# Optimization experiments

Hardware: AMD Instinct MI355X
Metric: run time of the kernel (lower is better)

Reference implementation:

```python
import jax, jax.numpy as jnp
import numpy as np

B, S, H, W, C = 1, 14, 56, 56, 192
WS = 7            # cubic window
SH = 3            # shift
HEADS = 6
HD = C // HEADS
N = WS ** 3       # 343 tokens per window
NW = (S // WS) * (H // WS) * (W // WS)  # 128 windows
SCALE = HD ** -0.5
HID = 4 * C
TBL = (2 * WS - 1) ** 3  # 2197


def _rel_index():
    # faithful to torch: meshgrid with indexing='xy' and the (3*ws-1)/(2*ws-1) strides
    c = np.stack(np.meshgrid(np.arange(WS), np.arange(WS), np.arange(WS), indexing='xy'))
    f = c.reshape(3, -1)                      # (3, N)
    r = (f[:, :, None] - f[:, None, :]).transpose(1, 2, 0)  # (N, N, 3)
    r = r + (WS - 1)
    r[..., 0] *= 3 * WS - 1
    r[..., 1] *= 2 * WS - 1
    return jnp.asarray(r.sum(-1), dtype=jnp.int32)  # (N, N)

REL_IDX = _rel_index()


def _ln(x, g, b):
    m = x.mean(-1, keepdims=True)
    v = ((x - m) ** 2).mean(-1, keepdims=True)
    return (x - m) * jax.lax.rsqrt(v + 1e-5) * g + b


def _partition(x):  # (B,S,H,W,C) -> (B*nW, N, C)
    x = x.reshape(B, S // WS, WS, H // WS, WS, W // WS, WS, C)
    x = x.transpose(0, 1, 3, 5, 2, 4, 6, 7)
    return x.reshape(-1, N, C)


def _reverse(w):  # (B*nW, N, C) -> (B,S,H,W,C)
    x = w.reshape(B, S // WS, H // WS, W // WS, WS, WS, WS, C)
    x = x.transpose(0, 1, 4, 2, 5, 3, 6, 7)
    return x.reshape(B, S, H, W, C)


def setup_inputs() -> dict:
    key = jax.random.key(0)
    ks = jax.random.split(key, 16)
    L = S * H * W
    p = lambda k, shp, s=0.02: (jax.random.normal(k, shp, dtype=jnp.float32) * s)
    return {
        'x': jax.random.normal(ks[0], (B, L, C), dtype=jnp.float32),
        'mask_matrix': jax.random.normal(ks[1], (NW, N, N), dtype=jnp.float32),
        'skip': jax.random.normal(ks[2], (B, L, C), dtype=jnp.float32),
        'x_up': jax.random.normal(ks[3], (B, L, C), dtype=jnp.float32),
        'norm1_g': jnp.ones((C,), jnp.float32),
        'norm1_b': jnp.zeros((C,), jnp.float32),
        'kv_w': p(ks[4], (C, 2 * C)),
        'kv_b': jnp.zeros((2 * C,), jnp.float32),
        'rel_bias_table': p(ks[5], (TBL, HEADS)),
        'proj_w': p(ks[6], (C, C)),
        'proj_b': jnp.zeros((C,), jnp.float32),
        'norm2_g': jnp.ones((C,), jnp.float32),
        'norm2_b': jnp.zeros((C,), jnp.float32),
        'fc1_w': p(ks[7], (C, HID)),
        'fc1_b': jnp.zeros((HID,), jnp.float32),
        'fc2_w': p(ks[8], (HID, C)),
        'fc2_b': jnp.zeros((C,), jnp.float32),
    }


def reference(x, mask_matrix, skip, x_up, norm1_g, norm1_b, kv_w, kv_b,
              rel_bias_table, proj_w, proj_b, norm2_g, norm2_b,
              fc1_w, fc1_b, fc2_w, fc2_b):
    shortcut = x
    sk = _ln(skip, norm1_g, norm1_b).reshape(B, S, H, W, C)
    xu = _ln(x_up, norm1_g, norm1_b).reshape(B, S, H, W, C)
    # cyclic shift (shift_size > 0, dims divisible by window -> no padding)
    sk = jnp.roll(sk, (-SH, -SH, -SH), axis=(1, 2, 3))
    xu = jnp.roll(xu, (-SH, -SH, -SH), axis=(1, 2, 3))
    sk_w = _partition(sk)   # (Bw, N, C)
    xu_w = _partition(xu)
    Bw = sk_w.shape[0]
    kv = (sk_w @ kv_w + kv_b).reshape(Bw, N, 2, HEADS, HD)
    k = kv[:, :, 0].transpose(0, 2, 1, 3)   # (Bw, h, N, d)
    v = kv[:, :, 1].transpose(0, 2, 1, 3)
    q = xu_w.reshape(Bw, N, HEADS, HD).transpose(0, 2, 1, 3) * SCALE
    attn = jnp.einsum('bhnd,bhmd->bhnm', q, k)
    bias = rel_bias_table[REL_IDX].transpose(2, 0, 1)  # (h, N, N)
    attn = attn + bias[None]
    attn = attn.reshape(B, NW, HEADS, N, N) + mask_matrix[None, :, None]
    attn = jax.nn.softmax(attn.reshape(Bw, HEADS, N, N), axis=-1)
    out = jnp.einsum('bhnm,bhmd->bhnd', attn, v)
    out = out.transpose(0, 2, 1, 3).reshape(Bw, N, C)
    out = out @ proj_w + proj_b
    xr = _reverse(out)
    xr = jnp.roll(xr, (SH, SH, SH), axis=(1, 2, 3)).reshape(B, S * H * W, C)
    x = shortcut + xr
    h = _ln(x, norm2_g, norm2_b)
    h = jax.nn.gelu(h @ fc1_w + fc1_b, approximate=False) @ fc2_w + fc2_b
    return x + h
```

## Files before the change

### kernel.cpp

```cpp
#include <hip/hip_runtime.h>
#include <cstddef>

typedef unsigned short u16;
typedef unsigned int   u32;
typedef __bf16 bf16_t;
typedef bf16_t bf16x8 __attribute__((ext_vector_type(8)));
typedef short  s16x4  __attribute__((ext_vector_type(4)));
typedef float  f32x4  __attribute__((ext_vector_type(4)));
typedef u16    u16x4  __attribute__((ext_vector_type(4)));

#define NPAD 352
#define VTS  352

__device__ __forceinline__ u16 f2b(float f) {
  return __builtin_bit_cast(u16, (__bf16)f);
}
__device__ __forceinline__ float b2f(u16 h) {
  return __uint_as_float(((u32)h) << 16);
}
__device__ __forceinline__ f32x4 mfma16(bf16x8 a, bf16x8 b, f32x4 c) {
  return __builtin_amdgcn_mfma_f32_16x16x32_bf16(a, b, c, 0, 0, 0);
}
__device__ __forceinline__ f32x4 mfma16x16(s16x4 a, s16x4 b, f32x4 c) {
#if __has_builtin(__builtin_amdgcn_mfma_f32_16x16x16bf16_1k)
  return __builtin_amdgcn_mfma_f32_16x16x16bf16_1k(a, b, c, 0, 0, 0);
#else
  f32x4 d;
  asm volatile("v_mfma_f32_16x16x16_bf16 %0, %1, %2, %3"
               : "=&v"(d) : "v"(a), "v"(b), "v"(c));
  return d;
#endif
}
__device__ __forceinline__ void gl_lds16(const void* g, void* l) {
  __builtin_amdgcn_global_load_lds((const __attribute__((address_space(1))) void*)g,
                                   (__attribute__((address_space(3))) void*)l, 16, 0, 0);
}

__device__ __forceinline__ int win_to_global(int w, int n) {
  int ws = w >> 6, wh = (w >> 3) & 7, ww = w & 7;
  int ts = (n * 1338) >> 16;
  int rem = n - ts * 49;
  int th = (rem * 9363) >> 16;
  int tw = rem - th * 7;
  int gs = ws * 7 + ts + 3; if (gs >= 14) gs -= 14;
  int gh = wh * 7 + th + 3; if (gh >= 56) gh -= 56;
  int gw = ww * 7 + tw + 3; if (gw >= 56) gw -= 56;
  return (gs * 56 + gh) * 56 + gw;
}

#define MC_END 15488
#define LN_END (MC_END + 10976)
#define WC_END (LN_END + 1824)
#define PRE_GRID (WC_END + 726)

__global__ __launch_bounds__(256) void k_pre(
    const float* __restrict__ mask, u16* __restrict__ mb,
    const float* __restrict__ skip, const float* __restrict__ xup,
    const float* __restrict__ g1, const float* __restrict__ b1,
    u16* __restrict__ skw, u16* __restrict__ qb,
    const float* __restrict__ kv_w, const float* __restrict__ proj_w,
    const float* __restrict__ fc1_w, const float* __restrict__ fc2_w,
    u16* kvT, u16* projT, u16* fc1T, u16* fc2T,
    const float* __restrict__ tbl, u16* __restrict__ bf) {
  int bid = blockIdx.x, tid = threadIdx.x;
  if (bid < MC_END) {
    int t = bid * 256 + tid;
    int w = t / (352 * 88);
    int r = t - w * (352 * 88);
    int n = r / 88;
    int q = r - n * 88;
    u16x4 v = {0, 0, 0, 0};
    if (n < 343) {
      const float* src = mask + ((size_t)w * 343 + n) * 343 + q * 4;
      #pragma unroll
      for (int j = 0; j < 4; ++j) if (q * 4 + j < 343) v[j] = f2b(src[j]);
    }
    *(u16x4*)&mb[((size_t)w * 352 + n) * 352 + q * 4] = v;
  } else if (bid < LN_END) {
    int wid = tid >> 6, lane = tid & 63;
    int m = (bid - MC_END) * 4 + wid;
    u32 w = ((u32)m * 48914u) >> 24;
    int n = m - (int)w * 343;
    int g = win_to_global((int)w, n);
    float xs[3], xu[3];
    float s1 = 0.f, s2 = 0.f, t1 = 0.f, t2 = 0.f;
    #pragma unroll
    for (int i = 0; i < 3; ++i) {
      int c = lane + i * 64;
      xs[i] = skip[(size_t)g * 192 + c];
      xu[i] = xup[(size_t)g * 192 + c];
      s1 += xs[i]; s2 += xs[i] * xs[i];
      t1 += xu[i]; t2 += xu[i] * xu[i];
    }
    #pragma unroll
    for (int off = 1; off < 64; off <<= 1) {
      s1 += __shfl_xor(s1, off); s2 += __shfl_xor(s2, off);
      t1 += __shfl_xor(t1, off); t2 += __shfl_xor(t2, off);
    }
    const float inv = 1.f / 192.f;
    float ms = s1 * inv, vs = s2 * inv - ms * ms;
    float mu = t1 * inv, vu = t2 * inv - mu * mu;
    float rs = rsqrtf(vs + 1e-5f), ru = rsqrtf(vu + 1e-5f);
    #pragma unroll
    for (int i = 0; i < 3; ++i) {
      int c = lane + i * 64;
      float gg = g1[c], bb = b1[c];
      skw[(size_t)m * 192 + c] = f2b((xs[i] - ms) * rs * gg + bb);
      float qv = ((xu[i] - mu) * ru * gg + bb) * 0.17677669529663687f;
      int h = c >> 5, d = c & 31;
      qb[(size_t)(((int)w * 6 + h) * NPAD + n) * 32 + d] = f2b(qv);
    }
  } else if (bid < WC_END) {
    int t = (bid - LN_END) * 256 + tid;
    if (t < 384 * 192) { int nn = t / 192, kk = t - nn * 192; kvT[t] = f2b(kv_w[kk * 384 + nn]); return; }
    t -= 384 * 192;
    if (t < 256 * 192) { int nn = t / 192, kk = t - nn * 192; projT[t] = (nn < 192) ? f2b(proj_w[kk * 192 + nn]) : (u16)0; return; }
    t -= 256 * 192;
    if (t < 768 * 192) { int nn = t / 192, kk = t - nn * 192; fc1T[t] = f2b(fc1_w[kk * 768 + nn]); return; }
    t -= 768 * 192;
    if (t < 256 * 768) { int nn = t / 768, kk = t - nn * 768; fc2T[t] = (nn < 192) ? f2b(fc2_w[kk * 192 + nn]) : (u16)0; return; }
  } else {
    int t = (bid - WC_END) * 256 + tid;
    int h = t / (352 * 88);
    int r = t - h * (352 * 88);
    int n = r / 88;
    int q = r - n * 88;
    u16x4 v = {0, 0, 0, 0};
    if (n < 343 && h < 6) {
      int tsn = (n * 1338) >> 16, remn = n - tsn * 49, thn = (remn * 9363) >> 16, twn = remn - thn * 7;
      #pragma unroll
      for (int j = 0; j < 4; ++j) {
        int m = q * 4 + j;
        if (m < 343) {
          int tsm = (m * 1338) >> 16, remm = m - tsm * 49, thm = (remm * 9363) >> 16, twm = remm - thm * 7;
          int idx = (thn - thm) * 20 + (tsn - tsm) * 13 + (twn - twm) + 204;
          v[j] = f2b(tbl[idx * 6 + h]);
        }
      }
    }
    if (h < 6) *(u16x4*)&bf[((size_t)h * 352 + n) * 352 + q * 4] = v;
  }
}

__global__ __launch_bounds__(256) void k_ln2(const float* __restrict__ xr,
    const float* __restrict__ g2, const float* __restrict__ b2, u16* __restrict__ o) {
  int wid = threadIdx.x >> 6, lane = threadIdx.x & 63;
  int m = blockIdx.x * 4 + wid;
  float v[3]; float s1 = 0.f, s2 = 0.f;
  #pragma unroll
  for (int i = 0; i < 3; ++i) {
    int c = lane + i * 64;
    v[i] = xr[(size_t)m * 192 + c];
    s1 += v[i]; s2 += v[i] * v[i];
  }
  #pragma unroll
  for (int off = 1; off < 64; off <<= 1) { s1 += __shfl_xor(s1, off); s2 += __shfl_xor(s2, off); }
  const float inv = 1.f / 192.f;
  float ms = s1 * inv, vs = s2 * inv - ms * ms;
  float rs = rsqrtf(vs + 1e-5f);
  #pragma unroll
  for (int i = 0; i < 3; ++i) {
    int c = lane + i * 64;
    o[(size_t)m * 192 + c] = f2b((v[i] - ms) * rs * g2[c] + b2[c]);
  }
}

template<int EPI>
__global__ __launch_bounds__(256) void k_gemm(
    const u16* __restrict__ A, const u16* __restrict__ Bm, int K, int nbn,
    const float* __restrict__ bias,
    u16* __restrict__ outa, u16* __restrict__ outb,
    const float* __restrict__ xin, float* __restrict__ xres,
    float* __restrict__ outf) {
  __shared__ __align__(16) u16 As[128 * 32];
  __shared__ __align__(16) u16 Bs[128 * 32];
  int bid = blockIdx.x;
  int xcd = bid & 7, j = bid >> 3;
  int bn = j % nbn, bmL = j / nbn;
  int bm = xcd * 43 + bmL;
  if (bm >= 343) return;
  int tid = threadIdx.x;
  int wid = tid >> 6, lane = tid & 63, lr = lane & 15, lg = lane >> 4;
  int wr = wid >> 1, wc = wid & 1;
  f32x4 acc[4][4] = {};
  const u16* Abase = A + (size_t)bm * 128 * K;
  const u16* Bbase = Bm + (size_t)bn * 128 * K;
  int nk = K >> 5;
  for (int kt = 0; kt < nk; ++kt) {
    int ci0 = tid, ci1 = tid + 256;
    int r0 = ci0 >> 2, c0 = (ci0 & 3) * 8;
    int r1 = ci1 >> 2, c1 = (ci1 & 3) * 8;
    gl_lds16(Abase + (size_t)r0 * K + kt * 32 + c0, &As[ci0 * 8]);
    gl_lds16(Abase + (size_t)r1 * K + kt * 32 + c1, &As[ci1 * 8]);
    gl_lds16(Bbase + (size_t)r0 * K + kt * 32 + c0, &Bs[ci0 * 8]);
    gl_lds16(Bbase + (size_t)r1 * K + kt * 32 + c1, &Bs[ci1 * 8]);
    __syncthreads();
    bf16x8 af[4], bfr[4];
    #pragma unroll
    for (int mi = 0; mi < 4; ++mi) af[mi] = *(const bf16x8*)&As[(wr * 64 + mi * 16 + lr) * 32 + lg * 8];
    #pragma unroll
    for (int ni = 0; ni < 4; ++ni) bfr[ni] = *(const bf16x8*)&Bs[(wc * 64 + ni * 16 + lr) * 32 + lg * 8];
    #pragma unroll
    for (int mi = 0; mi < 4; ++mi)
      #pragma unroll
      for (int ni = 0; ni < 4; ++ni)
        acc[mi][ni] = mfma16(af[mi], bfr[ni], acc[mi][ni]);
    __syncthreads();
  }
  #pragma unroll
  for (int mi = 0; mi < 4; ++mi) {
    #pragma unroll
    for (int r = 0; r < 4; ++r) {
      int grow = bm * 128 + wr * 64 + mi * 16 + lg * 4 + r;
      if (EPI == 0) {
        u32 w = ((u32)grow * 48914u) >> 24; int n = grow - (int)w * 343;
        #pragma unroll
        for (int ni = 0; ni < 4; ++ni) {
          int gcol = bn * 128 + wc * 64 + ni * 16 + lr;
          float v = acc[mi][ni][r] + bias[gcol];
          if (gcol < 192) {
            int hh = gcol >> 5, d = gcol & 31;
            int dswz = ((((d >> 3) ^ ((n >> 1) & 3)) << 3) | (d & 7));
            outa[(size_t)(((int)w * 6 + hh) * NPAD + n) * 32 + dswz] = f2b(v);
          } else {
            int c2 = gcol - 192; int hh = c2 >> 5, d = c2 & 31;
            int nswz = ((((n >> 3) ^ ((d >> 1) & 3)) << 3) | (n & 7));
            outb[(size_t)(((int)w * 6 + hh) * 32 + d) * VTS + nswz] = f2b(v);
          }
        }
      } else if (EPI == 1) {
        #pragma unroll
        for (int ni = 0; ni < 4; ++ni) {
          int gcol = bn * 128 + wc * 64 + ni * 16 + lr;
          if (gcol < 192) {
            float v = acc[mi][ni][r] + bias[gcol] + xin[(size_t)grow * 192 + gcol];
            xres[(size_t)grow * 192 + gcol] = v;
          }
        }
      } else if (EPI == 2) {
        #pragma unroll
        for (int ni = 0; ni < 4; ++ni) {
          int gcol = bn * 128 + wc * 64 + ni * 16 + lr;
          float v = acc[mi][ni][r] + bias[gcol];
          v = 0.5f * v * (1.f + erff(v * 0.7071067811865476f));
          outa[(size_t)grow * 768 + gcol] = f2b(v);
        }
      } else {
        #pragma unroll
        for (int ni = 0; ni < 4; ++ni) {
          int gcol = bn * 128 + wc * 64 + ni * 16 + lr;
          if (gcol < 192)
            outf[(size_t)grow * 192 + gcol] = acc[mi][ni][r] + bias[gcol] + xin[(size_t)grow * 192 + gcol];
        }
      }
    }
  }
}

template<int CT0, int LEN>
__device__ __forceinline__ void pf_load(const u16* __restrict__ brow, const u16* __restrict__ mrow,
                                        u16x4* bb, u16x4* mm) {
  #pragma unroll
  for (int j = 0; j < LEN; ++j) {
    bb[j] = *(const u16x4*)&brow[(CT0 + j) * 16];
    mm[j] = *(const u16x4*)&mrow[(CT0 + j) * 16];
  }
}

template<int CT0, int LEN, bool TAIL>
__device__ __forceinline__ void attn_chunk(const u16* __restrict__ Ks, const u16* __restrict__ Vs,
    bf16x8 qa, int lr, int lg, int swz, const u16x4* bb, const u16x4* mm,
    f32x4& o0, f32x4& o1, float& mrun, float& sum) {
  f32x4 s[LEN];
  const f32x4 z = {0.f, 0.f, 0.f, 0.f};
  __builtin_amdgcn_s_setprio(1);
  #pragma unroll
  for (int j = 0; j < LEN; ++j) {
    bf16x8 kf = *(const bf16x8*)&Ks[((CT0 + j) * 16 + lr) * 32 + (lg ^ swz) * 8];
    s[j] = mfma16(kf, qa, z);
  }
  __builtin_amdgcn_s_setprio(0);
  #pragma unroll
  for (int j = 0; j < LEN; ++j)
    #pragma unroll
    for (int r = 0; r < 4; ++r) s[j][r] += b2f(bb[j][r]) + b2f(mm[j][r]);
  if (TAIL) {
    int m0 = 336 + lg * 4;
    #pragma unroll
    for (int r = 0; r < 4; ++r) if (m0 + r >= 343) s[LEN - 1][r] = -1e30f;
  }
  float mloc = -1e30f;
  #pragma unroll
  for (int j = 0; j < LEN; ++j)
    mloc = fmaxf(mloc, fmaxf(fmaxf(s[j][0], s[j][1]), fmaxf(s[j][2], s[j][3])));
  mloc = fmaxf(mloc, __shfl_xor(mloc, 16));
  mloc = fmaxf(mloc, __shfl_xor(mloc, 32));
  float mnew = fmaxf(mrun, mloc);
  float scale = __expf(mrun - mnew);
  #pragma unroll
  for (int r = 0; r < 4; ++r) { o0[r] *= scale; o1[r] *= scale; }
  sum *= scale;
  float lsum = 0.f;
  #pragma unroll
  for (int j = 0; j < LEN; ++j)
    #pragma unroll
    for (int r = 0; r < 4; ++r) { float p = __expf(s[j][r] - mnew); s[j][r] = p; lsum += p; }
  lsum += __shfl_xor(lsum, 16);
  lsum += __shfl_xor(lsum, 32);
  sum += lsum;
  mrun = mnew;
  __builtin_amdgcn_s_setprio(1);
  #pragma unroll
  for (int j = 0; j < LEN; ++j) {
    s16x4 pa;
    #pragma unroll
    for (int r = 0; r < 4; ++r) pa[r] = (short)f2b(s[j][r]);
    int c16 = 2 * (CT0 + j) + (lg >> 1);
    int vo = ((c16 ^ swz) * 8) + (lg & 1) * 4;
    s16x4 v0 = *(const s16x4*)&Vs[lr * 352 + vo];
    s16x4 v1 = *(const s16x4*)&Vs[(16 + lr) * 352 + vo];
    o0 = mfma16x16(pa, v0, o0);
    o1 = mfma16x16(pa, v1, o1);
  }
  __builtin_amdgcn_s_setprio(0);
}

__global__ __launch_bounds__(256, 2) void k_attn(const u16* __restrict__ qb, const u16* __restrict__ kb,
    const u16* __restrict__ vtb, const u16* __restrict__ bfull, const u16* __restrict__ maskbf,
    u16* __restrict__ att) {
  __shared__ __align__(16) u16 Ks[352 * 32];
  __shared__ __align__(16) u16 Vs[32 * 352];
  __shared__ __align__(16) u16 Ot[4][16][40];
  int bid = blockIdx.x;
  int xcd = bid & 7, i = bid >> 3;
  int wl = i / 6, h = i - wl * 6;
  int w = xcd * 16 + wl;
  int tid = threadIdx.x, wid = tid >> 6, lane = tid & 63, lr = lane & 15, lg = lane >> 4;
  const u16* Q  = qb  + (size_t)(w * 6 + h) * NPAD * 32;
  const u16* Kg = kb  + (size_t)(w * 6 + h) * NPAD * 32;
  const u16* Vg = vtb + (size_t)(w * 6 + h) * 32 * VTS;
  const u16* Bp = bfull + (size_t)h * 352 * 352;
  const u16* Mp = maskbf + (size_t)w * 352 * 352;
  #pragma unroll
  for (int it = 0; it < 11; ++it) {
    int idx = it * 256 + tid;
    if (idx < 1408) gl_lds16(Kg + idx * 8, &Ks[idx * 8]);
    else            gl_lds16(Vg + (idx - 1408) * 8, &Vs[(idx - 1408) * 8]);
  }
  __syncthreads();
  int swz = (lr >> 1) & 3;
  for (int rt = wid; rt < 22; rt += 4) {
    int n = rt * 16 + lr;
    bf16x8 qa = *(const bf16x8*)&Q[(size_t)n * 32 + lg * 8];
    const u16* brow = Bp + (size_t)n * 352 + lg * 4;
    const u16* mrow = Mp + (size_t)n * 352 + lg * 4;
    f32x4 o0 = {0.f, 0.f, 0.f, 0.f}, o1 = {0.f, 0.f, 0.f, 0.f};
    float mrun = -1e30f, sum = 0.f;
    u16x4 bbA[6], mmA[6], bbB[6], mmB[6];
    pf_load<0, 6>(brow, mrow, bbA, mmA);
    pf_load<6, 6>(brow, mrow, bbB, mmB);
    attn_chunk<0, 6, false>(Ks, Vs, qa, lr, lg, swz, bbA, mmA, o0, o1, mrun, sum);
    pf_load<12, 6>(brow, mrow, bbA, mmA);
    attn_chunk<6, 6, false>(Ks, Vs, qa, lr, lg, swz, bbB, mmB, o0, o1, mrun, sum);
    pf_load<18, 4>(brow, mrow, bbB, mmB);
    attn_chunk<12, 6, false>(Ks, Vs, qa, lr, lg, swz, bbA, mmA, o0, o1, mrun, sum);
    attn_chunk<18, 4, true>(Ks, Vs, qa, lr, lg, swz, bbB, mmB, o0, o1, mrun, sum);
    float rs = 1.f / sum;
    #pragma unroll
    for (int r = 0; r < 4; ++r) {
      Ot[wid][lg * 4 + r][lr] = f2b(o0[r] * rs);
      Ot[wid][lg * 4 + r][16 + lr] = f2b(o1[r] * rs);
    }
    if (n < 343) {
      int g = win_to_global(w, n);
      bf16x8 ov = *(const bf16x8*)&Ot[wid][lr][lg * 8];
      *(bf16x8*)&att[(size_t)g * 192 + h * 32 + lg * 8] = ov;
    }
  }
}

static const size_t OFF_W    = 0;
static const size_t OFF_XRES = (size_t)1 << 20;
static const size_t OFF_MASK = OFF_XRES;
static const size_t OFF_LN2  = OFF_XRES + ((size_t)34 << 20);
static const size_t OFF_SKW  = OFF_LN2  + ((size_t)17 << 20);
static const size_t OFF_Q    = OFF_SKW  + ((size_t)17 << 20);
static const size_t OFF_K    = OFF_Q    + ((size_t)17 << 20);
static const size_t OFF_VT   = OFF_K    + ((size_t)17 << 20);
static const size_t OFF_ATT  = OFF_VT   + ((size_t)17 << 20);
static const size_t OFF_BIAS = OFF_ATT  + ((size_t)17 << 20);
static const size_t OFF_FC1  = OFF_SKW;

extern "C" void kernel_launch(void* const* d_in, const int* in_sizes, int n_in,
                              void* d_out, int out_size, void* d_ws, size_t ws_size,
                              hipStream_t stream) {
  const float* x      = (const float*)d_in[0];
  const float* mask   = (const float*)d_in[1];
  const float* skip   = (const float*)d_in[2];
  const float* xup    = (const float*)d_in[3];
  const float* n1g    = (const float*)d_in[4];
  const float* n1b    = (const float*)d_in[5];
  const float* kv_w   = (const float*)d_in[6];
  const float* kv_b   = (const float*)d_in[7];
  const float* tbl    = (const float*)d_in[8];
  const float* proj_w = (const float*)d_in[9];
  const float* proj_b = (const float*)d_in[10];
  const float* n2g    = (const float*)d_in[11];
  const float* n2b    = (const float*)d_in[12];
  const float* fc1_w  = (const float*)d_in[13];
  const float* fc1_b  = (const float*)d_in[14];
  const float* fc2_w  = (const float*)d_in[15];
  const float* fc2_b  = (const float*)d_in[16];
  char* ws = (char*)d_ws;
  u16* kvT   = (u16*)(ws + OFF_W);
  u16* projT = kvT + 384 * 192;
  u16* fc1T  = projT + 256 * 192;
  u16* fc2T  = fc1T + 768 * 192;
  float* xres = (float*)(ws + OFF_XRES);
  u16* maskbf = (u16*)(ws + OFF_MASK);
  u16* ln2o  = (u16*)(ws + OFF_LN2);
  u16* skw   = (u16*)(ws + OFF_SKW);
  u16* qb    = (u16*)(ws + OFF_Q);
  u16* kb    = (u16*)(ws + OFF_K);
  u16* vt    = (u16*)(ws + OFF_VT);
  u16* att   = (u16*)(ws + OFF_ATT);
  u16* bfull = (u16*)(ws + OFF_BIAS);
  u16* fc1o  = (u16*)(ws + OFF_FC1);
  float* outp = (float*)d_out;

  k_pre<<<dim3(PRE_GRID), dim3(256), 0, stream>>>(
      mask, maskbf, skip, xup, n1g, n1b, skw, qb,
      kv_w, proj_w, fc1_w, fc2_w, kvT, projT, fc1T, fc2T, tbl, bfull);
  k_gemm<0><<<dim3(8 * 43 * 3), dim3(256), 0, stream>>>(skw, kvT, 192, 3, kv_b, kb, vt, nullptr, nullptr, nullptr);
  k_attn<<<dim3(768), dim3(256), 0, stream>>>(qb, kb, vt, bfull, maskbf, att);
  k_gemm<1><<<dim3(8 * 43 * 2), dim3(256), 0, stream>>>(att, projT, 192, 2, proj_b, nullptr, nullptr, x, xres, nullptr);
  k_ln2<<<dim3(10976), dim3(256), 0, stream>>>(xres, n2g, n2b, ln2o);
  k_gemm<2><<<dim3(8 * 43 * 6), dim3(256), 0, stream>>>(ln2o, fc1T, 192, 6, fc1_b, fc1o, nullptr, nullptr, nullptr, nullptr);
  k_gemm<3><<<dim3(8 * 43 * 2), dim3(256), 0, stream>>>(fc1o, fc2T, 768, 2, fc2_b, nullptr, nullptr, xres, nullptr, outp);
}
```

Measured before the change: 317.9 us.

## Use exp2 softmax with pre-scaled logits and lazy rescaling in attention

Pre-multiplies q scale, relative bias and mask by log2(e) in the prep kernel so the attention softmax can use the native exp2 instruction. The online softmax skips the running-max rescale unless some new max exceeds the old one by a threshold, and defers the row-sum cross-lane reduction to the end. This cuts the exp arithmetic, shuffles and rescale multiplies in the inner chunk loop. In exchange, values can exceed the running max by up to 2^11.5 before a rescale, which loosens the fp32 headroom, and the output scaling now needs per-row shuffles.

```diff
diff --git a/kernel.cpp b/kernel.cpp
--- a/kernel.cpp
+++ b/kernel.cpp
@@ -11,12 +11,21 @@
 
 #define NPAD 352
 #define VTS  352
+#define LOG2E 1.4426950408889634f
+#define RESCALE_THR 11.5f
 
 __device__ __forceinline__ u16 f2b(float f) {
   return __builtin_bit_cast(u16, (__bf16)f);
 }
 __device__ __forceinline__ float b2f(u16 h) {
   return __uint_as_float(((u32)h) << 16);
+}
+__device__ __forceinline__ float fexp2(float x) {
+#if __has_builtin(__builtin_amdgcn_exp2f)
+  return __builtin_amdgcn_exp2f(x);
+#else
+  float r; asm("v_exp_f32 %0, %1" : "=v"(r) : "v"(x)); return r;
+#endif
 }
 __device__ __forceinline__ f32x4 mfma16(bf16x8 a, bf16x8 b, f32x4 c) {
   return __builtin_amdgcn_mfma_f32_16x16x32_bf16(a, b, c, 0, 0, 0);
@@ -73,7 +82,7 @@
     if (n < 343) {
       const float* src = mask + ((size_t)w * 343 + n) * 343 + q * 4;
       #pragma unroll
-      for (int j = 0; j < 4; ++j) if (q * 4 + j < 343) v[j] = f2b(src[j]);
+      for (int j = 0; j < 4; ++j) if (q * 4 + j < 343) v[j] = f2b(src[j] * LOG2E);
     }
     *(u16x4*)&mb[((size_t)w * 352 + n) * 352 + q * 4] = v;
   } else if (bid < LN_END) {
@@ -106,7 +115,7 @@
       int c = lane + i * 64;
       float gg = g1[c], bb = b1[c];
       skw[(size_t)m * 192 + c] = f2b((xs[i] - ms) * rs * gg + bb);
-      float qv = ((xu[i] - mu) * ru * gg + bb) * 0.17677669529663687f;
+      float qv = ((xu[i] - mu) * ru * gg + bb) * 0.25503513f;
       int h = c >> 5, d = c & 31;
       qb[(size_t)(((int)w * 6 + h) * NPAD + n) * 32 + d] = f2b(qv);
     }
@@ -134,7 +143,7 @@
         if (m < 343) {
           int tsm = (m * 1338) >> 16, remm = m - tsm * 49, thm = (remm * 9363) >> 16, twm = remm - thm * 7;
           int idx = (thn - thm) * 20 + (tsn - tsm) * 13 + (twn - twm) + 204;
-          v[j] = f2b(tbl[idx * 6 + h]);
+          v[j] = f2b(tbl[idx * 6 + h] * LOG2E);
         }
       }
     }
@@ -267,7 +276,7 @@
   }
 }
 
-template<int CT0, int LEN, bool TAIL>
+template<int CT0, int LEN, bool TAIL, bool FIRST>
 __device__ __forceinline__ void attn_chunk(const u16* __restrict__ Ks, const u16* __restrict__ Vs,
     bf16x8 qa, int lr, int lg, int swz, const u16x4* bb, const u16x4* mm,
     f32x4& o0, f32x4& o1, float& mrun, float& sum) {
@@ -293,22 +302,27 @@
   #pragma unroll
   for (int j = 0; j < LEN; ++j)
     mloc = fmaxf(mloc, fmaxf(fmaxf(s[j][0], s[j][1]), fmaxf(s[j][2], s[j][3])));
-  mloc = fmaxf(mloc, __shfl_xor(mloc, 16));
-  mloc = fmaxf(mloc, __shfl_xor(mloc, 32));
-  float mnew = fmaxf(mrun, mloc);
-  float scale = __expf(mrun - mnew);
-  #pragma unroll
-  for (int r = 0; r < 4; ++r) { o0[r] *= scale; o1[r] *= scale; }
-  sum *= scale;
-  float lsum = 0.f;
+  if (FIRST) {
+    mloc = fmaxf(mloc, __shfl_xor(mloc, 16));
+    mloc = fmaxf(mloc, __shfl_xor(mloc, 32));
+    mrun = mloc;
+  } else if (!__all(mloc <= mrun + RESCALE_THR)) {
+    mloc = fmaxf(mloc, __shfl_xor(mloc, 16));
+    mloc = fmaxf(mloc, __shfl_xor(mloc, 32));
+    float mnew = fmaxf(mrun, mloc);
+    float sc = fexp2(mrun - mnew);
+    #pragma unroll
+    for (int r = 0; r < 4; ++r) {
+      float scr = __shfl(sc, lg * 4 + r);
+      o0[r] *= scr; o1[r] *= scr;
+    }
+    sum *= sc;
+    mrun = mnew;
+  }
   #pragma unroll
   for (int j = 0; j < LEN; ++j)
     #pragma unroll
-    for (int r = 0; r < 4; ++r) { float p = __expf(s[j][r] - mnew); s[j][r] = p; lsum += p; }
-  lsum += __shfl_xor(lsum, 16);
-  lsum += __shfl_xor(lsum, 32);
-  sum += lsum;
-  mrun = mnew;
+    for (int r = 0; r < 4; ++r) { float p = fexp2(s[j][r] - mrun); s[j][r] = p; sum += p; }
   __builtin_amdgcn_s_setprio(1);
   #pragma unroll
   for (int j = 0; j < LEN; ++j) {
@@ -359,17 +373,20 @@
     u16x4 bbA[6], mmA[6], bbB[6], mmB[6];
     pf_load<0, 6>(brow, mrow, bbA, mmA);
     pf_load<6, 6>(brow, mrow, bbB, mmB);
-    attn_chunk<0, 6, false>(Ks, Vs, qa, lr, lg, swz, bbA, mmA, o0, o1, mrun, sum);
+    attn_chunk<0, 6, false, true >(Ks, Vs, qa, lr, lg, swz, bbA, mmA, o0, o1, mrun, sum);
     pf_load<12, 6>(brow, mrow, bbA, mmA);
-    attn_chunk<6, 6, false>(Ks, Vs, qa, lr, lg, swz, bbB, mmB, o0, o1, mrun, sum);
+    attn_chunk<6, 6, false, false>(Ks, Vs, qa, lr, lg, swz, bbB, mmB, o0, o1, mrun, sum);
     pf_load<18, 4>(brow, mrow, bbB, mmB);
-    attn_chunk<12, 6, false>(Ks, Vs, qa, lr, lg, swz, bbA, mmA, o0, o1, mrun, sum);
-    attn_chunk<18, 4, true>(Ks, Vs, qa, lr, lg, swz, bbB, mmB, o0, o1, mrun, sum);
+    attn_chunk<12, 6, false, false>(Ks, Vs, qa, lr, lg, swz, bbA, mmA, o0, o1, mrun, sum);
+    attn_chunk<18, 4, true, false>(Ks, Vs, qa, lr, lg, swz, bbB, mmB, o0, o1, mrun, sum);
+    sum += __shfl_xor(sum, 16);
+    sum += __shfl_xor(sum, 32);
     float rs = 1.f / sum;
     #pragma unroll
     for (int r = 0; r < 4; ++r) {
-      Ot[wid][lg * 4 + r][lr] = f2b(o0[r] * rs);
-      Ot[wid][lg * 4 + r][16 + lr] = f2b(o1[r] * rs);
+      float rsr = __shfl(rs, lg * 4 + r);
+      Ot[wid][lg * 4 + r][lr] = f2b(o0[r] * rsr);
+      Ot[wid][lg * 4 + r][16 + lr] = f2b(o1[r] * rsr);
     }
     if (n < 343) {
       int g = win_to_global(w, n);
```

Result: no change. 319.6 us (+0.5%).
